# Kernel tuning notes

Hardware: AMD Instinct MI355X
Metric: run time of the kernel (lower is better)

Reference implementation:

```python
import jax, jax.numpy as jnp
import numpy as np
import math

NUM_HEADS = 8
DIM_EMBED = 640
DIM_CROSS = 768
DIM_HEAD = DIM_EMBED // NUM_HEADS


def setup_inputs() -> dict:
    key = jax.random.key(0)
    ks = jax.random.split(key, 10)
    B, SQ, SKV = 32, 1024, 77
    s_e = 1.0 / math.sqrt(DIM_EMBED)
    s_c = 1.0 / math.sqrt(DIM_CROSS)
    return {
        "x": jax.random.normal(ks[0], (B, SQ, DIM_EMBED), jnp.float32),
        "y": jax.random.normal(ks[1], (B, SKV, DIM_CROSS), jnp.float32),
        "Wq": jax.random.normal(ks[2], (DIM_EMBED, DIM_EMBED), jnp.float32) * s_e,
        "bq": jax.random.normal(ks[3], (DIM_EMBED,), jnp.float32) * 0.01,
        "Wk": jax.random.normal(ks[4], (DIM_CROSS, DIM_EMBED), jnp.float32) * s_c,
        "bk": jax.random.normal(ks[5], (DIM_EMBED,), jnp.float32) * 0.01,
        "Wv": jax.random.normal(ks[6], (DIM_CROSS, DIM_EMBED), jnp.float32) * s_c,
        "bv": jax.random.normal(ks[7], (DIM_EMBED,), jnp.float32) * 0.01,
        "Wo": jax.random.normal(ks[8], (DIM_EMBED, DIM_EMBED), jnp.float32) * s_e,
        "bo": jax.random.normal(ks[9], (DIM_EMBED,), jnp.float32) * 0.01,
    }


def reference(x, y, Wq, bq, Wk, bk, Wv, bv, Wo, bo):
    B, SQ, E = x.shape
    H, D = NUM_HEADS, DIM_HEAD
    q = x @ Wq + bq                      # [B, SQ, E]
    k = y @ Wk + bk                      # [B, SKV, E]
    v = y @ Wv + bv                      # [B, SKV, E]
    q = q.reshape(B, SQ, H, D)
    k = k.reshape(B, -1, H, D)
    v = v.reshape(B, -1, H, D)
    scores = jnp.einsum("bqhd,bkhd->bhqk", q, k) / math.sqrt(D)
    w = jax.nn.softmax(scores, axis=-1)
    out = jnp.einsum("bhqk,bkhd->bqhd", w, v).reshape(B, SQ, E)
    return out @ Wo + bo
```

## Files before the change

kernel.cpp:

```cpp
#include <hip/hip_runtime.h>
#include <hip/hip_bf16.h>

typedef __bf16 bf16x8 __attribute__((ext_vector_type(8)));
typedef float f32x4 __attribute__((ext_vector_type(4)));
typedef unsigned short us8 __attribute__((ext_vector_type(8)));
typedef unsigned int u32x4 __attribute__((ext_vector_type(4)));

#define E_ 640
#define CD_ 768
#define B_ 32
#define SQ_ 1024
#define SKV_ 77
#define H_ 8
#define DH_ 80

typedef __attribute__((address_space(3))) unsigned int as3_u32;
typedef __attribute__((address_space(1))) const unsigned int as1_u32;

__device__ __forceinline__ void gload16(const unsigned short* g, unsigned short* l) {
    __builtin_amdgcn_global_load_lds((as1_u32*)g, (as3_u32*)l, 16, 0, 0);
}
__device__ __forceinline__ void gload16f(const float* g, unsigned short* l) {
    __builtin_amdgcn_global_load_lds((as1_u32*)g, (as3_u32*)l, 16, 0, 0);
}

__device__ __forceinline__ float b2f(unsigned short u) {
    unsigned int x = ((unsigned int)u) << 16;
    return __builtin_bit_cast(float, x);
}
__device__ __forceinline__ unsigned short f2b(float f) {
    unsigned int x = __builtin_bit_cast(unsigned int, f);
    x += 0x7fffu + ((x >> 16) & 1u);
    return (unsigned short)(x >> 16);
}
__device__ __forceinline__ bf16x8 lv8(const unsigned short* p) {
    return __builtin_bit_cast(bf16x8, *reinterpret_cast<const us8*>(p));
}
__device__ __forceinline__ bf16x8 zero8() {
    us8 z = {0,0,0,0,0,0,0,0};
    return __builtin_bit_cast(bf16x8, z);
}
__device__ __forceinline__ us8 cvt8(const float* s) {
    f32x4 f0 = *reinterpret_cast<const f32x4*>(s);
    f32x4 f1 = *reinterpret_cast<const f32x4*>(s + 4);
    us8 v;
    v[0]=f2b(f0[0]); v[1]=f2b(f0[1]); v[2]=f2b(f0[2]); v[3]=f2b(f0[3]);
    v[4]=f2b(f1[0]); v[5]=f2b(f1[1]); v[6]=f2b(f1[2]); v[7]=f2b(f1[3]);
    return v;
}
__device__ __forceinline__ bf16x8 cvtpk8(f32x4 lo, f32x4 hi) {
    unsigned int w0, w1, w2, w3;
    asm("v_cvt_pk_bf16_f32 %0, %1, %2" : "=v"(w0) : "v"(lo[0]), "v"(lo[1]));
    asm("v_cvt_pk_bf16_f32 %0, %1, %2" : "=v"(w1) : "v"(lo[2]), "v"(lo[3]));
    asm("v_cvt_pk_bf16_f32 %0, %1, %2" : "=v"(w2) : "v"(hi[0]), "v"(hi[1]));
    asm("v_cvt_pk_bf16_f32 %0, %1, %2" : "=v"(w3) : "v"(hi[2]), "v"(hi[3]));
    u32x4 w = {w0, w1, w2, w3};
    return __builtin_bit_cast(bf16x8, w);
}

__device__ __forceinline__ void transpose_body(
    const float* __restrict__ in, unsigned short* __restrict__ out,
    int K, int N, int bx, int by, unsigned short (*t)[33])
{
    const int tx = threadIdx.x & 31, ty = threadIdx.x >> 5;
    const int n0 = bx * 32, k0 = by * 32;
#pragma unroll
    for (int i = 0; i < 4; ++i)
        t[ty + 8*i][tx] = f2b(in[(size_t)(k0 + ty + 8*i) * N + n0 + tx]);
    __syncthreads();
#pragma unroll
    for (int i = 0; i < 4; ++i)
        out[(size_t)(n0 + ty + 8*i) * K + k0 + tx] = t[tx][ty + 8*i];
}

__global__ __launch_bounds__(256) void fused_prep(
    const float* __restrict__ Wq, unsigned short* __restrict__ WqT,
    const float* __restrict__ Wo, unsigned short* __restrict__ WoT,
    const float* __restrict__ Wk, unsigned short* __restrict__ WkT,
    const float* __restrict__ Wv, unsigned short* __restrict__ WvT)
{
    __shared__ unsigned short t[32][33];
    const int id = blockIdx.x;
    if (id < 800) {
        int z = id / 400, rem = id % 400;
        transpose_body(z ? Wo : Wq, z ? WoT : WqT, 640, 640, rem % 20, rem / 20, t);
    } else {
        int id2 = id - 800, z = id2 / 480, rem = id2 % 480;
        transpose_body(z ? Wv : Wk, z ? WvT : WkT, 768, 640, rem % 20, rem / 20, t);
    }
}

template<int AMODE, bool CF32>
__device__ __forceinline__ void gemm_body(
    const void* __restrict__ Ap,
    const unsigned short* __restrict__ Wt,
    const float* __restrict__ bias,
    void* __restrict__ Cp,
    int M, int K, int ldc, int m0, int n0,
    unsigned short* smem)
{
    constexpr int BUFSTRIDE = (AMODE == 2) ? 12288 : 8192;
    constexpr int AWOFF     = (AMODE == 2) ? 8192 : 4096;
    const int tid = threadIdx.x, lane = tid & 63, wave = tid >> 6;
    const int wr = (wave >> 1) << 6, wc = (wave & 1) << 6;
    const int l15 = lane & 15, l4 = lane >> 4;

    const int cw = wave * 64 + lane;
    const unsigned short* gW0 = Wt + (size_t)(n0 + (cw >> 2)) * K + (cw & 3) * 8;
    const unsigned short* gW1 = Wt + (size_t)(n0 + ((cw + 256) >> 2)) * K + ((cw + 256) & 3) * 8;

    const unsigned short* gA0; const unsigned short* gA1;
    const float* fA0; const float* fA1;
    const float* xbase; int aoff[4];
    if constexpr (AMODE == 0) {
        gA0 = (const unsigned short*)Ap + (size_t)(m0 + (cw >> 2)) * K + (cw & 3) * 8;
        gA1 = (const unsigned short*)Ap + (size_t)(m0 + ((cw + 256) >> 2)) * K + ((cw + 256) & 3) * 8;
    } else if constexpr (AMODE == 1) {
        int c0 = tid, c1 = tid + 256;
        int r0 = m0 + (c0 >> 2); if (r0 >= M) r0 = M - 1;
        int r1 = m0 + (c1 >> 2); if (r1 >= M) r1 = M - 1;
        fA0 = (const float*)Ap + (size_t)r0 * K + (c0 & 3) * 8;
        fA1 = (const float*)Ap + (size_t)r1 * K + (c1 & 3) * 8;
    } else {
        xbase = (const float*)Ap + (size_t)m0 * K;
#pragma unroll
        for (int j = 0; j < 4; ++j) {
            int c = j * 256 + tid;
            int row = c >> 3, sg = (c & 7) ^ (row & 7);
            aoff[j] = row * K + sg * 4;
        }
    }

    f32x4 acc[4][4];
#pragma unroll
    for (int m = 0; m < 4; ++m)
#pragma unroll
        for (int n = 0; n < 4; ++n)
#pragma unroll
            for (int i = 0; i < 4; ++i) acc[m][n][i] = 0.f;

    auto STAGE = [&](int buf) {
        unsigned short* As = smem + buf * BUFSTRIDE;
        unsigned short* Ws = As + AWOFF;
        if constexpr (AMODE == 0) {
            gload16(gA0, As + cw * 8);
            gload16(gA1, As + (cw + 256) * 8);
            gA0 += 32; gA1 += 32;
        } else if constexpr (AMODE == 1) {
            *reinterpret_cast<us8*>(As + tid * 8) = cvt8(fA0);
            *reinterpret_cast<us8*>(As + (tid + 256) * 8) = cvt8(fA1);
            fA0 += 32; fA1 += 32;
        } else {
#pragma unroll
            for (int j = 0; j < 4; ++j)
                gload16f(xbase + aoff[j], As + (j * 256 + tid) * 8);
            xbase += 32;
        }
        gload16(gW0, Ws + cw * 8);
        gload16(gW1, Ws + (cw + 256) * 8);
        gW0 += 32; gW1 += 32;
    };
    auto COMPUTE = [&](int buf) {
        const unsigned short* As = smem + buf * BUFSTRIDE;
        const unsigned short* Ws = As + AWOFF;
        bf16x8 a[4], b[4];
        if constexpr (AMODE == 2) {
            const float* Af = (const float*)As;
#pragma unroll
            for (int m = 0; m < 4; ++m) {
                const int row = wr + m * 16 + l15;
                const int t0 = (l4 * 2) ^ (row & 7);
                const int t1 = (l4 * 2 + 1) ^ (row & 7);
                f32x4 lo = *reinterpret_cast<const f32x4*>(Af + row * 32 + t0 * 4);
                f32x4 hi = *reinterpret_cast<const f32x4*>(Af + row * 32 + t1 * 4);
                a[m] = cvtpk8(lo, hi);
            }
        } else {
#pragma unroll
            for (int m = 0; m < 4; ++m)
                a[m] = lv8(&As[(wr + m * 16 + l15) * 32 + l4 * 8]);
        }
#pragma unroll
        for (int n = 0; n < 4; ++n)
            b[n] = lv8(&Ws[(wc + n * 16 + l15) * 32 + l4 * 8]);
        __builtin_amdgcn_s_setprio(1);
#pragma unroll
        for (int m = 0; m < 4; ++m)
#pragma unroll
            for (int n = 0; n < 4; ++n)
                acc[m][n] = __builtin_amdgcn_mfma_f32_16x16x32_bf16(a[m], b[n], acc[m][n], 0, 0, 0);
        __builtin_amdgcn_s_setprio(0);
    };

    const int nk = K >> 5;
    STAGE(0);
    __syncthreads();
    for (int kt = 0; kt < nk - 2; kt += 2) {
        STAGE(1);
        COMPUTE(0);
        __syncthreads();
        STAGE(0);
        COMPUTE(1);
        __syncthreads();
    }
    STAGE(1);
    COMPUTE(0);
    __syncthreads();
    COMPUTE(1);

    float bs[4];
#pragma unroll
    for (int n = 0; n < 4; ++n) bs[n] = bias[n0 + wc + n * 16 + l15];

    if constexpr (CF32) {
        float* C = (float*)Cp;
        float* fs = (float*)smem;
#pragma unroll
        for (int p = 0; p < 2; ++p) {
            __syncthreads();
            if (wr == p * 64) {
#pragma unroll
                for (int m = 0; m < 4; ++m)
#pragma unroll
                    for (int n = 0; n < 4; ++n)
#pragma unroll
                        for (int i = 0; i < 4; ++i)
                            fs[(m * 16 + l4 * 4 + i) * 128 + wc + n * 16 + l15] =
                                acc[m][n][i] + bs[n];
            }
            __syncthreads();
#pragma unroll
            for (int r = 0; r < 8; ++r) {
                const int off = (r * 256 + tid) * 4;
                const int row = off >> 7, col = off & 127;
                const int grow = m0 + p * 64 + row;
                if (grow < M)
                    *reinterpret_cast<f32x4*>(&C[(size_t)grow * ldc + n0 + col]) =
                        *reinterpret_cast<const f32x4*>(&fs[off]);
            }
        }
    } else {
        unsigned short* C = (unsigned short*)Cp;
#pragma unroll
        for (int p = 0; p < 2; ++p) {
            __syncthreads();
            if (wr == p * 64) {
#pragma unroll
                for (int m = 0; m < 4; ++m)
#pragma unroll
                    for (int n = 0; n < 4; ++n)
#pragma unroll
                        for (int i = 0; i < 4; ++i)
                            smem[(m * 16 + l4 * 4 + i) * 128 + wc + n * 16 + l15] =
                                f2b(acc[m][n][i] + bs[n]);
            }
            __syncthreads();
#pragma unroll
            for (int r = 0; r < 4; ++r) {
                const int off = (r * 256 + tid) * 8;
                const int row = off >> 7, col = off & 127;
                const int grow = m0 + p * 64 + row;
                if (grow < M)
                    *reinterpret_cast<us8*>(&C[(size_t)grow * ldc + n0 + col]) =
                        *reinterpret_cast<us8*>(&smem[off]);
            }
        }
    }
}

__global__ __launch_bounds__(256) void gemm_o(
    const unsigned short* __restrict__ Ap, const unsigned short* __restrict__ Wt,
    const float* __restrict__ bias, float* __restrict__ Cp)
{
    __shared__ __align__(16) unsigned short smem[16384];
    const int orig = blockIdx.x;
    const int wgid = (orig & 7) * 160 + (orig >> 3);
    gemm_body<0, true>(Ap, Wt, bias, Cp, 32768, 640, 640, (wgid / 5) * 128, (wgid % 5) * 128, smem);
}

__global__ __launch_bounds__(256) void fused_qkv(
    const float* __restrict__ x, const unsigned short* __restrict__ WqT,
    const float* __restrict__ bq, unsigned short* __restrict__ Qb,
    const float* __restrict__ y,
    const unsigned short* __restrict__ WkT, const float* __restrict__ bk2, unsigned short* __restrict__ Kb,
    const unsigned short* __restrict__ WvT, const float* __restrict__ bv2, unsigned short* __restrict__ Vb)
{
    __shared__ __align__(16) unsigned short smem[24576];
    const int id = blockIdx.x;
    if (id < 200) {
        int z = id / 100, rem = id % 100;
        int m0 = (rem / 5) * 128, n0 = (rem % 5) * 128;
        if (z == 0) gemm_body<1, false>(y, WkT, bk2, Kb, 2464, 768, 640, m0, n0, smem);
        else        gemm_body<1, false>(y, WvT, bv2, Vb, 2464, 768, 640, m0, n0, smem);
    } else {
        int orig = id - 200;
        int wgid = (orig & 7) * 160 + (orig >> 3);
        int m0 = (wgid / 5) * 128, n0 = (wgid % 5) * 128;
        gemm_body<2, false>(x, WqT, bq, Qb, 32768, 640, 640, m0, n0, smem);
    }
}

__global__ __launch_bounds__(256) void vtrans_kernel(
    const unsigned short* __restrict__ Vb, unsigned short* __restrict__ Vt)
{
    __shared__ unsigned short Vl[77 * 88 + 8];
    const int b = blockIdx.x, h = blockIdx.y;
    const int tid = threadIdx.x;
    for (int idx = tid; idx < 770; idx += 256) {
        int kv = idx / 10, seg = idx % 10;
        *reinterpret_cast<us8*>(&Vl[kv * 88 + seg * 8]) =
            *reinterpret_cast<const us8*>(&Vb[(size_t)(b * 77 + kv) * 640 + h * 80 + seg * 8]);
    }
    __syncthreads();
    unsigned short* out = Vt + (size_t)(b * 8 + h) * 6400;
    for (int idx = tid; idx < 800; idx += 256) {
        int d = idx / 10, seg = idx % 10;
        us8 v;
#pragma unroll
        for (int j = 0; j < 8; ++j) {
            int kv = seg * 8 + j;
            v[j] = (kv < 77) ? Vl[kv * 88 + d] : (unsigned short)0;
        }
        *reinterpret_cast<us8*>(&out[d * 80 + seg * 8]) = v;
    }
}

__global__ __launch_bounds__(128) void attn_kernel(
    const unsigned short* __restrict__ Q,
    const unsigned short* __restrict__ Kp,
    const unsigned short* __restrict__ Vt,
    unsigned short* __restrict__ Oa)
{
    __shared__ __align__(16) unsigned short smem[11272];
    const int tid = threadIdx.x, lane = tid & 63, wave = tid >> 6;
    const int l15 = lane & 15, l4 = lane >> 4;
    const int qb = blockIdx.x * 128, h = blockIdx.y, b = blockIdx.z;
    const size_t qrow0 = (size_t)b * SQ_ + qb + wave * 64;
    const size_t kbase = (size_t)b * SKV_ * E_ + h * DH_;
    const size_t vbase = (size_t)(b * 8 + h) * 6400;

    bf16x8 aq[3][4];
#pragma unroll
    for (int ks = 0; ks < 3; ++ks) {
        const int d = ks * 32 + l4 * 8;
#pragma unroll
        for (int m = 0; m < 4; ++m)
            aq[ks][m] = (d < 80) ? lv8(&Q[(qrow0 + m * 16 + l15) * E_ + h * DH_ + d]) : zero8();
    }

    f32x4 accS[4][5];
#pragma unroll
    for (int m = 0; m < 4; ++m)
#pragma unroll
        for (int n = 0; n < 5; ++n)
#pragma unroll
            for (int i = 0; i < 4; ++i) accS[m][n][i] = 0.f;

#pragma unroll
    for (int ks = 0; ks < 3; ++ks) {
        const int d = ks * 32 + l4 * 8;
        bf16x8 bk[5];
#pragma unroll
        for (int n = 0; n < 5; ++n) {
            const int kv = n * 16 + l15;
            bk[n] = (kv < SKV_ && d < 80) ? lv8(&Kp[kbase + (size_t)kv * E_ + d]) : zero8();
        }
        __builtin_amdgcn_s_setprio(1);
#pragma unroll
        for (int n = 0; n < 5; ++n)
#pragma unroll
            for (int m = 0; m < 4; ++m)
                accS[m][n] = __builtin_amdgcn_mfma_f32_16x16x32_bf16(aq[ks][m], bk[n], accS[m][n], 0, 0, 0);
        __builtin_amdgcn_s_setprio(0);
    }

    unsigned short* Pw = smem + wave * 5632;

    const float scale = 0.11180339887498949f;
    float rs[4][4];
#pragma unroll
    for (int m = 0; m < 4; ++m) {
#pragma unroll
        for (int i = 0; i < 4; ++i) {
            float mx = -1e30f;
#pragma unroll
            for (int n = 0; n < 5; ++n) {
                float s = accS[m][n][i] * scale;
                if (n == 4 && l15 >= 13) s = -1e30f;
                accS[m][n][i] = s;
                mx = fmaxf(mx, s);
            }
            mx = fmaxf(mx, __shfl_xor(mx, 1));
            mx = fmaxf(mx, __shfl_xor(mx, 2));
            mx = fmaxf(mx, __shfl_xor(mx, 4));
            mx = fmaxf(mx, __shfl_xor(mx, 8));
            float sum = 0.f;
            const int prow = m * 16 + l4 * 4 + i;
#pragma unroll
            for (int n = 0; n < 5; ++n) {
                float p = __expf(accS[m][n][i] - mx);
                sum += p;
                Pw[prow * 88 + n * 16 + l15] = f2b(p);
            }
            sum += __shfl_xor(sum, 1);
            sum += __shfl_xor(sum, 2);
            sum += __shfl_xor(sum, 4);
            sum += __shfl_xor(sum, 8);
            rs[m][i] = sum;
        }
    }

    f32x4 accO[4][5];
#pragma unroll
    for (int m = 0; m < 4; ++m)
#pragma unroll
        for (int n = 0; n < 5; ++n)
#pragma unroll
            for (int i = 0; i < 4; ++i) accO[m][n][i] = 0.f;

#pragma unroll
    for (int ks = 0; ks < 3; ++ks) {
        const int kv = ks * 32 + l4 * 8;
        bf16x8 ap[4], bv[5];
#pragma unroll
        for (int m = 0; m < 4; ++m)
            ap[m] = (ks < 2 || l4 < 2) ? lv8(&Pw[(m * 16 + l15) * 88 + ks * 32 + l4 * 8])
                                       : zero8();
#pragma unroll
        for (int n = 0; n < 5; ++n) {
            const int d = n * 16 + l15;
            bv[n] = (kv < 80) ? lv8(&Vt[vbase + (size_t)d * 80 + kv]) : zero8();
        }
        __builtin_amdgcn_s_setprio(1);
#pragma unroll
        for (int n = 0; n < 5; ++n)
#pragma unroll
            for (int m = 0; m < 4; ++m)
                accO[m][n] = __builtin_amdgcn_mfma_f32_16x16x32_bf16(ap[m], bv[n], accO[m][n], 0, 0, 0);
        __builtin_amdgcn_s_setprio(0);
    }

    __syncthreads();
#pragma unroll
    for (int m = 0; m < 4; ++m) {
#pragma unroll
        for (int i = 0; i < 4; ++i) {
            const float inv = 1.f / rs[m][i];
            const int rl = wave * 64 + m * 16 + l4 * 4 + i;
#pragma unroll
            for (int n = 0; n < 5; ++n)
                smem[rl * 80 + n * 16 + l15] = f2b(accO[m][n][i] * inv);
        }
    }
    __syncthreads();
    const size_t obase = (size_t)b * SQ_ + qb;
    for (int idx = tid; idx < 1280; idx += 128) {
        int row = idx / 10, seg = idx % 10;
        *reinterpret_cast<us8*>(&Oa[(obase + row) * E_ + h * DH_ + seg * 8]) =
            *reinterpret_cast<us8*>(&smem[row * 80 + seg * 8]);
    }
}

extern "C" void kernel_launch(void* const* d_in, const int* in_sizes, int n_in,
                              void* d_out, int out_size, void* d_ws, size_t ws_size,
                              hipStream_t stream) {
    const float* x  = (const float*)d_in[0];
    const float* y  = (const float*)d_in[1];
    const float* Wq = (const float*)d_in[2];
    const float* bq = (const float*)d_in[3];
    const float* Wk = (const float*)d_in[4];
    const float* bk = (const float*)d_in[5];
    const float* Wv = (const float*)d_in[6];
    const float* bv = (const float*)d_in[7];
    const float* Wo = (const float*)d_in[8];
    const float* bo = (const float*)d_in[9];
    float* out = (float*)d_out;

    char* ws = (char*)d_ws;
    unsigned short* WqT = (unsigned short*)(ws + 0);
    unsigned short* WkT = (unsigned short*)(ws + 819200);
    unsigned short* WvT = (unsigned short*)(ws + 1802240);
    unsigned short* WoT = (unsigned short*)(ws + 2785280);
    unsigned short* Qb  = (unsigned short*)(ws + 3604480);
    unsigned short* Kb  = (unsigned short*)(ws + 45547520);
    unsigned short* Vb  = (unsigned short*)(ws + 48701440);
    unsigned short* Vtb = (unsigned short*)(ws + 51855360);

    fused_prep<<<1760, 256, 0, stream>>>(Wq, WqT, Wo, WoT, Wk, WkT, Wv, WvT);
    fused_qkv<<<1480, 256, 0, stream>>>(x, WqT, bq, Qb, y, WkT, bk, Kb, WvT, bv, Vb);
    vtrans_kernel<<<dim3(32, 8), 256, 0, stream>>>(Vb, Vtb);
    attn_kernel<<<dim3(8, 8, 32), 128, 0, stream>>>(Qb, Kb, Vtb, Qb);
    gemm_o<<<1280, 256, 0, stream>>>(Qb, WoT, bo, out);
}
```

Baseline: 166.4 us.

## Load GEMM A operand directly from global into registers, stage only weights in LDS

The A operand of all projection GEMMs is now loaded straight from global memory into registers, one k-tile ahead, instead of being staged through LDS. Only the weight tile still goes through LDS with double buffering. The fp32 inputs (x, y) are converted to bf16 in registers just before the MFMAs, and the Q/K/V kernel's LDS allocation shrinks to match. This removes LDS traffic and footprint for A and may raise occupancy, but the two waves sharing a row band now load the same A data twice, and the per-lane row-strided global loads are less coalesced.

```diff
diff --git a/kernel.cpp b/kernel.cpp
--- a/kernel.cpp
+++ b/kernel.cpp
@@ -20,9 +20,6 @@
 __device__ __forceinline__ void gload16(const unsigned short* g, unsigned short* l) {
     __builtin_amdgcn_global_load_lds((as1_u32*)g, (as3_u32*)l, 16, 0, 0);
 }
-__device__ __forceinline__ void gload16f(const float* g, unsigned short* l) {
-    __builtin_amdgcn_global_load_lds((as1_u32*)g, (as3_u32*)l, 16, 0, 0);
-}
 
 __device__ __forceinline__ float b2f(unsigned short u) {
     unsigned int x = ((unsigned int)u) << 16;
@@ -39,14 +36,6 @@
 __device__ __forceinline__ bf16x8 zero8() {
     us8 z = {0,0,0,0,0,0,0,0};
     return __builtin_bit_cast(bf16x8, z);
-}
-__device__ __forceinline__ us8 cvt8(const float* s) {
-    f32x4 f0 = *reinterpret_cast<const f32x4*>(s);
-    f32x4 f1 = *reinterpret_cast<const f32x4*>(s + 4);
-    us8 v;
-    v[0]=f2b(f0[0]); v[1]=f2b(f0[1]); v[2]=f2b(f0[2]); v[3]=f2b(f0[3]);
-    v[4]=f2b(f1[0]); v[5]=f2b(f1[1]); v[6]=f2b(f1[2]); v[7]=f2b(f1[3]);
-    return v;
 }
 __device__ __forceinline__ bf16x8 cvtpk8(f32x4 lo, f32x4 hi) {
     unsigned int w0, w1, w2, w3;
@@ -99,8 +88,6 @@
     int M, int K, int ldc, int m0, int n0,
     unsigned short* smem)
 {
-    constexpr int BUFSTRIDE = (AMODE == 2) ? 12288 : 8192;
-    constexpr int AWOFF     = (AMODE == 2) ? 8192 : 4096;
     const int tid = threadIdx.x, lane = tid & 63, wave = tid >> 6;
     const int wr = (wave >> 1) << 6, wc = (wave & 1) << 6;
     const int l15 = lane & 15, l4 = lane >> 4;
@@ -109,26 +96,11 @@
     const unsigned short* gW0 = Wt + (size_t)(n0 + (cw >> 2)) * K + (cw & 3) * 8;
     const unsigned short* gW1 = Wt + (size_t)(n0 + ((cw + 256) >> 2)) * K + ((cw + 256) & 3) * 8;
 
-    const unsigned short* gA0; const unsigned short* gA1;
-    const float* fA0; const float* fA1;
-    const float* xbase; int aoff[4];
-    if constexpr (AMODE == 0) {
-        gA0 = (const unsigned short*)Ap + (size_t)(m0 + (cw >> 2)) * K + (cw & 3) * 8;
-        gA1 = (const unsigned short*)Ap + (size_t)(m0 + ((cw + 256) >> 2)) * K + ((cw + 256) & 3) * 8;
-    } else if constexpr (AMODE == 1) {
-        int c0 = tid, c1 = tid + 256;
-        int r0 = m0 + (c0 >> 2); if (r0 >= M) r0 = M - 1;
-        int r1 = m0 + (c1 >> 2); if (r1 >= M) r1 = M - 1;
-        fA0 = (const float*)Ap + (size_t)r0 * K + (c0 & 3) * 8;
-        fA1 = (const float*)Ap + (size_t)r1 * K + (c1 & 3) * 8;
-    } else {
-        xbase = (const float*)Ap + (size_t)m0 * K;
-#pragma unroll
-        for (int j = 0; j < 4; ++j) {
-            int c = j * 256 + tid;
-            int row = c >> 3, sg = (c & 7) ^ (row & 7);
-            aoff[j] = row * K + sg * 4;
-        }
+    size_t arow[4];
+#pragma unroll
+    for (int m = 0; m < 4; ++m) {
+        int r = m0 + wr + m * 16 + l15; if (r >= M) r = M - 1;
+        arow[m] = (size_t)r * K;
     }
 
     f32x4 acc[4][4];
@@ -140,46 +112,14 @@
             for (int i = 0; i < 4; ++i) acc[m][n][i] = 0.f;
 
     auto STAGE = [&](int buf) {
-        unsigned short* As = smem + buf * BUFSTRIDE;
-        unsigned short* Ws = As + AWOFF;
-        if constexpr (AMODE == 0) {
-            gload16(gA0, As + cw * 8);
-            gload16(gA1, As + (cw + 256) * 8);
-            gA0 += 32; gA1 += 32;
-        } else if constexpr (AMODE == 1) {
-            *reinterpret_cast<us8*>(As + tid * 8) = cvt8(fA0);
-            *reinterpret_cast<us8*>(As + (tid + 256) * 8) = cvt8(fA1);
-            fA0 += 32; fA1 += 32;
-        } else {
-#pragma unroll
-            for (int j = 0; j < 4; ++j)
-                gload16f(xbase + aoff[j], As + (j * 256 + tid) * 8);
-            xbase += 32;
-        }
+        unsigned short* Ws = smem + buf * 4096;
         gload16(gW0, Ws + cw * 8);
         gload16(gW1, Ws + (cw + 256) * 8);
         gW0 += 32; gW1 += 32;
     };
-    auto COMPUTE = [&](int buf) {
-        const unsigned short* As = smem + buf * BUFSTRIDE;
-        const unsigned short* Ws = As + AWOFF;
-        bf16x8 a[4], b[4];
-        if constexpr (AMODE == 2) {
-            const float* Af = (const float*)As;
-#pragma unroll
-            for (int m = 0; m < 4; ++m) {
-                const int row = wr + m * 16 + l15;
-                const int t0 = (l4 * 2) ^ (row & 7);
-                const int t1 = (l4 * 2 + 1) ^ (row & 7);
-                f32x4 lo = *reinterpret_cast<const f32x4*>(Af + row * 32 + t0 * 4);
-                f32x4 hi = *reinterpret_cast<const f32x4*>(Af + row * 32 + t1 * 4);
-                a[m] = cvtpk8(lo, hi);
-            }
-        } else {
-#pragma unroll
-            for (int m = 0; m < 4; ++m)
-                a[m] = lv8(&As[(wr + m * 16 + l15) * 32 + l4 * 8]);
-        }
+    auto COMPUTE = [&](int buf, bf16x8 (&a)[4]) {
+        const unsigned short* Ws = smem + buf * 4096;
+        bf16x8 b[4];
 #pragma unroll
         for (int n = 0; n < 4; ++n)
             b[n] = lv8(&Ws[(wc + n * 16 + l15) * 32 + l4 * 8]);
@@ -193,20 +133,54 @@
     };
 
     const int nk = K >> 5;
-    STAGE(0);
-    __syncthreads();
-    for (int kt = 0; kt < nk - 2; kt += 2) {
-        STAGE(1);
-        COMPUTE(0);
+
+    if constexpr (AMODE == 3) {
+        const unsigned short* A = (const unsigned short*)Ap;
+        auto LOADA = [&](int kt, bf16x8 (&a)[4]) {
+#pragma unroll
+            for (int m = 0; m < 4; ++m)
+                a[m] = lv8(A + arow[m] + kt * 32 + l4 * 8);
+        };
+        bf16x8 aA[4], aB[4];
+        LOADA(0, aA); STAGE(0);
         __syncthreads();
-        STAGE(0);
-        COMPUTE(1);
+        for (int kt = 0; kt < nk - 2; kt += 2) {
+            LOADA(kt + 1, aB); STAGE(1); COMPUTE(0, aA);
+            __syncthreads();
+            LOADA(kt + 2, aA); STAGE(0); COMPUTE(1, aB);
+            __syncthreads();
+        }
+        LOADA(nk - 1, aB); STAGE(1); COMPUTE(0, aA);
         __syncthreads();
-    }
-    STAGE(1);
-    COMPUTE(0);
-    __syncthreads();
-    COMPUTE(1);
+        COMPUTE(1, aB);
+    } else {
+        const float* A = (const float*)Ap;
+        auto LOADA = [&](int kt, f32x4 (&lo)[4], f32x4 (&hi)[4]) {
+#pragma unroll
+            for (int m = 0; m < 4; ++m) {
+                const float* p = A + arow[m] + kt * 32 + l4 * 8;
+                lo[m] = *reinterpret_cast<const f32x4*>(p);
+                hi[m] = *reinterpret_cast<const f32x4*>(p + 4);
+            }
+        };
+        auto CVT = [&](f32x4 (&lo)[4], f32x4 (&hi)[4], bf16x8 (&a)[4]) {
+#pragma unroll
+            for (int m = 0; m < 4; ++m) a[m] = cvtpk8(lo[m], hi[m]);
+        };
+        f32x4 loA[4], hiA[4], loB[4], hiB[4];
+        bf16x8 am[4];
+        LOADA(0, loA, hiA); STAGE(0);
+        __syncthreads();
+        for (int kt = 0; kt < nk - 2; kt += 2) {
+            LOADA(kt + 1, loB, hiB); STAGE(1); CVT(loA, hiA, am); COMPUTE(0, am);
+            __syncthreads();
+            LOADA(kt + 2, loA, hiA); STAGE(0); CVT(loB, hiB, am); COMPUTE(1, am);
+            __syncthreads();
+        }
+        LOADA(nk - 1, loB, hiB); STAGE(1); CVT(loA, hiA, am); COMPUTE(0, am);
+        __syncthreads();
+        CVT(loB, hiB, am); COMPUTE(1, am);
+    }
 
     float bs[4];
 #pragma unroll
@@ -275,7 +249,7 @@
     __shared__ __align__(16) unsigned short smem[16384];
     const int orig = blockIdx.x;
     const int wgid = (orig & 7) * 160 + (orig >> 3);
-    gemm_body<0, true>(Ap, Wt, bias, Cp, 32768, 640, 640, (wgid / 5) * 128, (wgid % 5) * 128, smem);
+    gemm_body<3, true>(Ap, Wt, bias, Cp, 32768, 640, 640, (wgid / 5) * 128, (wgid % 5) * 128, smem);
 }
 
 __global__ __launch_bounds__(256) void fused_qkv(
@@ -285,18 +259,18 @@
     const unsigned short* __restrict__ WkT, const float* __restrict__ bk2, unsigned short* __restrict__ Kb,
     const unsigned short* __restrict__ WvT, const float* __restrict__ bv2, unsigned short* __restrict__ Vb)
 {
-    __shared__ __align__(16) unsigned short smem[24576];
+    __shared__ __align__(16) unsigned short smem[8192];
     const int id = blockIdx.x;
     if (id < 200) {
         int z = id / 100, rem = id % 100;
         int m0 = (rem / 5) * 128, n0 = (rem % 5) * 128;
-        if (z == 0) gemm_body<1, false>(y, WkT, bk2, Kb, 2464, 768, 640, m0, n0, smem);
-        else        gemm_body<1, false>(y, WvT, bv2, Vb, 2464, 768, 640, m0, n0, smem);
+        if (z == 0) gemm_body<4, false>(y, WkT, bk2, Kb, 2464, 768, 640, m0, n0, smem);
+        else        gemm_body<4, false>(y, WvT, bv2, Vb, 2464, 768, 640, m0, n0, smem);
     } else {
         int orig = id - 200;
         int wgid = (orig & 7) * 160 + (orig >> 3);
         int m0 = (wgid / 5) * 128, n0 = (wgid % 5) * 128;
-        gemm_body<2, false>(x, WqT, bq, Qb, 32768, 640, 640, m0, n0, smem);
+        gemm_body<4, false>(x, WqT, bq, Qb, 32768, 640, 640, m0, n0, smem);
     }
 }
 
```

Result: slower. 245.3 us (+47.5%).
